# Performance work log

Measured on AMD Instinct MI355X. Metric: run time of the kernel, lower is better.

## Reference

```python
import jax, jax.numpy as jnp
import numpy as np

EPS = 1e-5
N0, K1, K2 = 1000, 500, 100  # node counts fixed by the view() calls in the source


def _conv_bn_relu(x, w, b, g, be):
    # Conv1d(k=1) == per-node linear; BatchNorm1d in training mode over nodes
    h = x @ w.T + b                      # (N, Cout)
    mu = h.mean(0)
    var = h.var(0)                       # biased variance, as torch BN uses
    return jax.nn.relu(g * (h - mu) * jax.lax.rsqrt(var + EPS) + be)


def _linear_relu(x, w, b):
    return jax.nn.relu(x @ w.T + b)


def _sag_pool(x, src, dst, ew, w_rel, w_root, bias, k):
    # SAGPooling with GraphConv scorer (sum aggregation weighted by edge_attr)
    N = x.shape[0]
    agg = jax.ops.segment_sum(ew[:, None] * x[src], dst, num_segments=N)  # (N, C)
    score = agg @ w_rel + x @ w_root + bias                               # (N,)
    top_s, perm = jax.lax.top_k(score, k)
    xk = x[perm] * jnp.tanh(top_s)[:, None]                               # (k, C)
    # re-index edges: keep only edges between surviving nodes (mask, fixed E)
    new_idx = jnp.zeros(N, jnp.int32).at[perm].set(jnp.arange(k, dtype=jnp.int32))
    keep = jnp.zeros(N, bool).at[perm].set(True)
    valid = keep[src] & keep[dst]
    nsrc = jnp.where(valid, new_idx[src], 0)
    ndst = jnp.where(valid, new_idx[dst], 0)
    new_ew = jnp.where(valid, ew, 0.0)  # zero weight == edge removed
    return xk, nsrc, ndst, new_ew


def setup_inputs() -> dict:
    key = jax.random.key(0)
    ks = jax.random.split(key, 32)
    nrm = lambda k, sh, s=0.05: jax.random.normal(k, sh, jnp.float32) * s
    E = 32000
    return {
        "x": jax.random.normal(ks[0], (1, N0, 3), jnp.float32),
        "edge_index": jax.random.randint(ks[1], (2, E), 0, N0, jnp.int32),
        "edge_attr": jax.random.uniform(ks[2], (E,), jnp.float32),
        # input: Conv1d(3,64)+BN
        "w0": nrm(ks[3], (64, 3)), "b0": jnp.zeros(64), "g0": jnp.ones(64), "be0": jnp.zeros(64),
        # mlp_first: Conv1d(64,64)+BN
        "w1": nrm(ks[4], (64, 64)), "b1": jnp.zeros(64), "g1": jnp.ones(64), "be1": jnp.zeros(64),
        # mlp_second: Conv1d(64,128)+BN, Conv1d(128,200)+BN
        "w2a": nrm(ks[5], (128, 64)), "b2a": jnp.zeros(128), "g2a": jnp.ones(128), "be2a": jnp.zeros(128),
        "w2b": nrm(ks[6], (200, 128)), "b2b": jnp.zeros(200), "g2b": jnp.ones(200), "be2b": jnp.zeros(200),
        # mlp_third: Conv1d(200,128), Conv1d(128,2) (no BN)
        "w3a": nrm(ks[7], (128, 200)), "b3a": jnp.zeros(128),
        "w3b": nrm(ks[8], (2, 128)), "b3b": jnp.zeros(2),
        # SAGPooling scorers (GraphConv(in_channels, 1))
        "p1_wrel": nrm(ks[9], (64,)), "p1_wroot": nrm(ks[10], (64,)), "p1_b": jnp.zeros(()),
        "p2_wrel": nrm(ks[11], (200,)), "p2_wroot": nrm(ks[12], (200,)), "p2_b": jnp.zeros(()),
    }


def reference(x, edge_index, edge_attr,
              w0, b0, g0, be0, w1, b1, g1, be1,
              w2a, b2a, g2a, be2a, w2b, b2b, g2b, be2b,
              w3a, b3a, w3b, b3b,
              p1_wrel, p1_wroot, p1_b, p2_wrel, p2_wroot, p2_b):
    h = x.reshape(N0, 3)
    src, dst = edge_index[0], edge_index[1]
    ew = edge_attr.reshape(-1)

    h = _conv_bn_relu(h, w0, b0, g0, be0)      # (1000, 64)
    h = _conv_bn_relu(h, w1, b1, g1, be1)      # (1000, 64)
    h, src, dst, ew = _sag_pool(h, src, dst, ew, p1_wrel, p1_wroot, p1_b, K1)

    h = _conv_bn_relu(h, w2a, b2a, g2a, be2a)  # (500, 128)
    h = _conv_bn_relu(h, w2b, b2b, g2b, be2b)  # (500, 200)
    h, src, dst, ew = _sag_pool(h, src, dst, ew, p2_wrel, p2_wroot, p2_b, K2)

    g = h.max(0)                               # global max pool over 100 nodes -> (200,)
    h3 = _linear_relu(g, w3a, b3a)             # (128,)
    out = _linear_relu(h3, w3b, b3b)           # (2,)
    return jax.nn.log_softmax(out)[None, :]    # (1, 2)
```

## Files before the change

### kernel.cpp

```cpp
#include <hip/hip_runtime.h>
#include <math.h>

#define EPS 1e-5f
#define N0 1000
#define NK1 500
#define NK2 100
#define NE 32000
#define NBLK 64

__device__ __forceinline__ float bnr(float h, float sc, float sh) {
    float v = fmaf(h, sc, sh);
    return v > 0.f ? v : 0.f;
}

__device__ __forceinline__ float aload(const float* p) {
    return __hip_atomic_load(p, __ATOMIC_RELAXED, __HIP_MEMORY_SCOPE_AGENT);
}
__device__ __forceinline__ void astore(float* p, float v) {
    __hip_atomic_store(p, v, __ATOMIC_RELAXED, __HIP_MEMORY_SCOPE_AGENT);
}
__device__ __forceinline__ int aiload(const int* p) {
    return __hip_atomic_load(p, __ATOMIC_RELAXED, __HIP_MEMORY_SCOPE_AGENT);
}
__device__ __forceinline__ void aistore(int* p, int v) {
    __hip_atomic_store(p, v, __ATOMIC_RELAXED, __HIP_MEMORY_SCOPE_AGENT);
}

__device__ __forceinline__ void gsync(unsigned* bar, unsigned k) {
    asm volatile("s_waitcnt vmcnt(0) lgkmcnt(0)" ::: "memory");
    __syncthreads();
    if (threadIdx.x == 0) {
        __hip_atomic_fetch_add(bar, 1u, __ATOMIC_RELAXED, __HIP_MEMORY_SCOPE_AGENT);
        const unsigned target = NBLK * k;
        unsigned spins = 0;
        while (__hip_atomic_load(bar, __ATOMIC_RELAXED, __HIP_MEMORY_SCOPE_AGENT) < target) {
            if (++spins > (1u << 20)) break;
            __builtin_amdgcn_s_sleep(1);
        }
    }
    __syncthreads();
}

struct Args {
    const float *x; const int *ei; const float *ea;
    const float *w0, *b0, *g0, *be0;
    const float *w1, *b1, *g1, *be1;
    const float *w2a, *b2a, *g2a, *be2a;
    const float *w2b, *b2b, *g2b, *be2b;
    const float *w3a, *b3a, *w3b, *b3b;
    const float *p1_wrel, *p1_wroot, *p1_b, *p2_wrel, *p2_wroot, *p2_b;
    float *h1, *psum1, *sc1, *t1, *xp1, *h2a, *psum2a;
    float *h2b, *psum2b, *t2, *sc2, *xp2;
    int *rk_g, *nsrc, *ndst; float *new_ew;
    unsigned *bar;
    float *out;
};

__global__ __launch_bounds__(256) void k_mega(Args a) {
    union __align__(16) SMem {
        struct { float xs[32][68], wsm[64][65], rs[256], rq[256], sc0[64], sh0[64]; } m1;
        struct { float xs[16][68], wsm[128][65], rs[256], rq[256]; } m2;
        struct { float wsm[200][33], xs[8][36], sc[128], sh[128]; } m3;
        struct { float acc[N0]; } sct;
        struct { float ss[N0], sc[200], sh[200]; } rk;
        struct { float sc[200], sh[200]; } bn;
        struct { float g[200], h3[128], o[2]; } fin;
    };
    __shared__ SMem sm;
    const int b = blockIdx.x, t = threadIdx.x;
    const int lane = t & 63, wv = t >> 6;

    if (b < 32) {
        const int c = lane, slot = wv;
        const int nb = b * 32;
        {
            float wa = a.w0[c * 3], wb = a.w0[c * 3 + 1], wc = a.w0[c * 3 + 2], bb = a.b0[c];
            float s = 0.f, q = 0.f;
            for (int n = slot; n < N0; n += 4) {
                float h = fmaf(wa, a.x[n * 3], fmaf(wb, a.x[n * 3 + 1], fmaf(wc, a.x[n * 3 + 2], bb)));
                s += h; q += h * h;
            }
            sm.m1.rs[t] = s; sm.m1.rq[t] = q;
            __syncthreads();
            if (t < 64) {
                float S = sm.m1.rs[t] + sm.m1.rs[t + 64] + sm.m1.rs[t + 128] + sm.m1.rs[t + 192];
                float Q = sm.m1.rq[t] + sm.m1.rq[t + 64] + sm.m1.rq[t + 128] + sm.m1.rq[t + 192];
                float mu = S * (1.f / N0);
                float var = Q * (1.f / N0) - mu * mu;
                float sv = a.g0[t] * rsqrtf(var + EPS);
                sm.m1.sc0[t] = sv; sm.m1.sh0[t] = a.be0[t] - mu * sv;
            }
            __syncthreads();
        }
        for (int i = 0; i < 8; ++i) {
            int e = t + i * 256;
            int r = e >> 6, cc = e & 63;
            int n = nb + r;
            float v = 0.f;
            if (n < N0) {
                float h = fmaf(a.w0[cc * 3], a.x[n * 3],
                          fmaf(a.w0[cc * 3 + 1], a.x[n * 3 + 1],
                          fmaf(a.w0[cc * 3 + 2], a.x[n * 3 + 2], a.b0[cc])));
                v = bnr(h, sm.m1.sc0[cc], sm.m1.sh0[cc]);
            }
            sm.m1.xs[r][cc] = v;
        }
        for (int i = 0; i < 16; ++i) {
            int e = t + i * 256;
            sm.m1.wsm[e >> 6][e & 63] = a.w1[e];
        }
        __syncthreads();
        float sacc = 0.f, qacc = 0.f;
        float bb1 = a.b1[c];
        for (int g = 0; g < 2; ++g) {
            int r0 = slot * 8 + g * 4;
            float a0 = bb1, a1 = bb1, a2 = bb1, a3 = bb1;
            #pragma unroll
            for (int kq = 0; kq < 16; ++kq) {
                float w0v = sm.m1.wsm[c][4 * kq], w1v = sm.m1.wsm[c][4 * kq + 1];
                float w2v = sm.m1.wsm[c][4 * kq + 2], w3v = sm.m1.wsm[c][4 * kq + 3];
                float4 x0 = *(const float4*)&sm.m1.xs[r0 + 0][4 * kq];
                float4 x1 = *(const float4*)&sm.m1.xs[r0 + 1][4 * kq];
                float4 x2 = *(const float4*)&sm.m1.xs[r0 + 2][4 * kq];
                float4 x3 = *(const float4*)&sm.m1.xs[r0 + 3][4 * kq];
                a0 = fmaf(x0.x, w0v, fmaf(x0.y, w1v, fmaf(x0.z, w2v, fmaf(x0.w, w3v, a0))));
                a1 = fmaf(x1.x, w0v, fmaf(x1.y, w1v, fmaf(x1.z, w2v, fmaf(x1.w, w3v, a1))));
                a2 = fmaf(x2.x, w0v, fmaf(x2.y, w1v, fmaf(x2.z, w2v, fmaf(x2.w, w3v, a2))));
                a3 = fmaf(x3.x, w0v, fmaf(x3.y, w1v, fmaf(x3.z, w2v, fmaf(x3.w, w3v, a3))));
            }
            float av[4] = {a0, a1, a2, a3};
            #pragma unroll
            for (int i = 0; i < 4; ++i) {
                int n = nb + r0 + i;
                if (n < N0) {
                    astore(&a.h1[n * 64 + c], av[i]);
                    sacc += av[i]; qacc += av[i] * av[i];
                }
            }
        }
        sm.m1.rs[t] = sacc; sm.m1.rq[t] = qacc;
        __syncthreads();
        if (t < 64) {
            astore(&a.psum1[b * 128 + t],      sm.m1.rs[t] + sm.m1.rs[t + 64] + sm.m1.rs[t + 128] + sm.m1.rs[t + 192]);
            astore(&a.psum1[b * 128 + 64 + t], sm.m1.rq[t] + sm.m1.rq[t + 64] + sm.m1.rq[t + 128] + sm.m1.rq[t + 192]);
        }
    }
    gsync(a.bar, 1);

    if (b < 63) {
        if (t < 64) {
            float s = 0.f, q = 0.f;
            for (int i = 0; i < 32; ++i) { s += aload(&a.psum1[i * 128 + t]); q += aload(&a.psum1[i * 128 + 64 + t]); }
            float mu = s * (1.f / N0);
            float var = q * (1.f / N0) - mu * mu;
            float sv = a.g1[t] * rsqrtf(var + EPS);
            sm.bn.sc[t] = sv; sm.bn.sh[t] = a.be1[t] - mu * sv;
        }
        __syncthreads();
        for (int it = 0; it < 4; ++it) {
            int n = b * 16 + it * 4 + wv;
            if (n < N0) {
                float v = bnr(aload(&a.h1[n * 64 + lane]), sm.bn.sc[lane], sm.bn.sh[lane]);
                float dr = v * a.p1_wrel[lane], dt = v * a.p1_wroot[lane];
                #pragma unroll
                for (int m = 32; m >= 1; m >>= 1) {
                    dr += __shfl_xor(dr, m, 64);
                    dt += __shfl_xor(dt, m, 64);
                }
                if (lane == 0) { astore(&a.t1[n], dr); astore(&a.sc1[n], dt + a.p1_b[0]); }
            }
        }
    }
    gsync(a.bar, 2);

    if (b < 16) {
        for (int i = t; i < N0; i += 256) sm.sct.acc[i] = 0.f;
        __syncthreads();
        for (int e = b * 256 + t; e < NE; e += 16 * 256) {
            float w = a.ea[e];
            if (w != 0.f) atomicAdd(&sm.sct.acc[a.ei[NE + e]], w * aload(&a.t1[a.ei[e]]));
        }
        __syncthreads();
        for (int i = t; i < N0; i += 256) {
            float v = sm.sct.acc[i];
            if (v != 0.f) atomicAdd(&a.sc1[i], v);
        }
    }
    gsync(a.bar, 3);

    if (b < 63) {
        if (t < 64) {
            float s = 0.f, q = 0.f;
            for (int i = 0; i < 32; ++i) { s += aload(&a.psum1[i * 128 + t]); q += aload(&a.psum1[i * 128 + 64 + t]); }
            float mu = s * (1.f / N0);
            float var = q * (1.f / N0) - mu * mu;
            float sv = a.g1[t] * rsqrtf(var + EPS);
            sm.rk.sc[t] = sv; sm.rk.sh[t] = a.be1[t] - mu * sv;
        }
        for (int i = t; i < N0; i += 256) sm.rk.ss[i] = aload(&a.sc1[i]);
        __syncthreads();
        for (int it = 0; it < 4; ++it) {
            int n = b * 16 + it * 4 + wv;
            if (n < N0) {
                float s = sm.rk.ss[n];
                int r = 0;
                for (int m = lane; m < N0; m += 64) {
                    float smv = sm.rk.ss[m];
                    r += (smv > s) || (smv == s && m < n);
                }
                #pragma unroll
                for (int msk = 32; msk >= 1; msk >>= 1) r += __shfl_xor(r, msk, 64);
                if (lane == 0) aistore(&a.rk_g[n], r);
                if (r < NK1) {
                    float tn = tanhf(s);
                    astore(&a.xp1[r * 64 + lane],
                           bnr(aload(&a.h1[n * 64 + lane]), sm.rk.sc[lane], sm.rk.sh[lane]) * tn);
                }
            }
        }
    }
    gsync(a.bar, 4);

    if (b < 32) {
        const int nb = b * 16;
        const int nrows = (NK1 - nb) < 16 ? (NK1 - nb) : 16;
        for (int i = 0; i < 4; ++i) {
            int e = t + i * 256;
            int r = e >> 6, cc = e & 63;
            sm.m2.xs[r][cc] = (r < nrows) ? aload(&a.xp1[(nb + r) * 64 + cc]) : 0.f;
        }
        for (int i = 0; i < 32; ++i) {
            int e = t + i * 256;
            sm.m2.wsm[e >> 6][e & 63] = a.w2a[e];
        }
        __syncthreads();
        const int c = t & 127, slot = t >> 7;
        float sacc = 0.f, qacc = 0.f;
        float bb2 = a.b2a[c];
        for (int g = 0; g < 2; ++g) {
            int r0 = slot * 8 + g * 4;
            float a0 = bb2, a1 = bb2, a2 = bb2, a3 = bb2;
            #pragma unroll
            for (int kq = 0; kq < 16; ++kq) {
                float w0v = sm.m2.wsm[c][4 * kq], w1v = sm.m2.wsm[c][4 * kq + 1];
                float w2v = sm.m2.wsm[c][4 * kq + 2], w3v = sm.m2.wsm[c][4 * kq + 3];
                float4 x0 = *(const float4*)&sm.m2.xs[r0 + 0][4 * kq];
                float4 x1 = *(const float4*)&sm.m2.xs[r0 + 1][4 * kq];
                float4 x2 = *(const float4*)&sm.m2.xs[r0 + 2][4 * kq];
                float4 x3 = *(const float4*)&sm.m2.xs[r0 + 3][4 * kq];
                a0 = fmaf(x0.x, w0v, fmaf(x0.y, w1v, fmaf(x0.z, w2v, fmaf(x0.w, w3v, a0))));
                a1 = fmaf(x1.x, w0v, fmaf(x1.y, w1v, fmaf(x1.z, w2v, fmaf(x1.w, w3v, a1))));
                a2 = fmaf(x2.x, w0v, fmaf(x2.y, w1v, fmaf(x2.z, w2v, fmaf(x2.w, w3v, a2))));
                a3 = fmaf(x3.x, w0v, fmaf(x3.y, w1v, fmaf(x3.z, w2v, fmaf(x3.w, w3v, a3))));
            }
            float av[4] = {a0, a1, a2, a3};
            #pragma unroll
            for (int i = 0; i < 4; ++i) {
                int r = r0 + i;
                if (r < nrows) {
                    astore(&a.h2a[(nb + r) * 128 + c], av[i]);
                    sacc += av[i]; qacc += av[i] * av[i];
                }
            }
        }
        sm.m2.rs[t] = sacc; sm.m2.rq[t] = qacc;
        __syncthreads();
        if (t < 128) {
            astore(&a.psum2a[b * 256 + t],       sm.m2.rs[t] + sm.m2.rs[t + 128]);
            astore(&a.psum2a[b * 256 + 128 + t], sm.m2.rq[t] + sm.m2.rq[t + 128]);
        }
    } else {
        int e0 = (b - 32) * 1000;
        for (int e = e0 + t; e < e0 + 1000; e += 256) {
            int s_ = a.ei[e], d_ = a.ei[NE + e];
            int rs_ = aiload(&a.rk_g[s_]), rd_ = aiload(&a.rk_g[d_]);
            bool v = (rs_ < NK1) && (rd_ < NK1);
            aistore(&a.nsrc[e], v ? rs_ : 0);
            aistore(&a.ndst[e], v ? rd_ : 0);
            astore(&a.new_ew[e], v ? a.ea[e] : 0.f);
        }
    }
    gsync(a.bar, 5);

    {
        const int nb = b * 8;
        if (nb < NK1) {
            const int nrows = (NK1 - nb) < 8 ? (NK1 - nb) : 8;
            if (t < 128) {
                float s = 0.f, q = 0.f;
                for (int i = 0; i < 32; ++i) { s += aload(&a.psum2a[i * 256 + t]); q += aload(&a.psum2a[i * 256 + 128 + t]); }
                float mu = s * (1.f / NK1);
                float var = q * (1.f / NK1) - mu * mu;
                float sv = a.g2a[t] * rsqrtf(var + EPS);
                sm.m3.sc[t] = sv; sm.m3.sh[t] = a.be2a[t] - mu * sv;
            }
            float acc[8];
            float bb = (t < 200) ? a.b2b[t] : 0.f;
            #pragma unroll
            for (int r = 0; r < 8; ++r) acc[r] = bb;
            for (int kt = 0; kt < 4; ++kt) {
                int k0 = kt * 32;
                __syncthreads();
                for (int i = 0; i < 25; ++i) {
                    int e = t + i * 256;
                    int r = e >> 5, k = e & 31;
                    sm.m3.wsm[r][k] = a.w2b[r * 128 + k0 + k];
                }
                {
                    int r = t >> 5, k = t & 31;
                    sm.m3.xs[r][k] = (r < nrows)
                        ? bnr(aload(&a.h2a[(nb + r) * 128 + k0 + k]), sm.m3.sc[k0 + k], sm.m3.sh[k0 + k]) : 0.f;
                }
                __syncthreads();
                if (t < 200) {
                    #pragma unroll
                    for (int kq = 0; kq < 8; ++kq) {
                        float w0v = sm.m3.wsm[t][4 * kq], w1v = sm.m3.wsm[t][4 * kq + 1];
                        float w2v = sm.m3.wsm[t][4 * kq + 2], w3v = sm.m3.wsm[t][4 * kq + 3];
                        #pragma unroll
                        for (int r = 0; r < 8; ++r) {
                            float4 xv = *(const float4*)&sm.m3.xs[r][4 * kq];
                            acc[r] = fmaf(xv.x, w0v, fmaf(xv.y, w1v, fmaf(xv.z, w2v, fmaf(xv.w, w3v, acc[r]))));
                        }
                    }
                }
            }
            if (t < 200) {
                float s = 0.f, q = 0.f;
                #pragma unroll
                for (int r = 0; r < 8; ++r) {
                    if (r < nrows) {
                        astore(&a.h2b[(nb + r) * 200 + t], acc[r]);
                        s += acc[r]; q += acc[r] * acc[r];
                    }
                }
                astore(&a.psum2b[b * 400 + t], s);
                astore(&a.psum2b[b * 400 + 200 + t], q);
            }
        } else if (t < 200) {
            astore(&a.psum2b[b * 400 + t], 0.f);
            astore(&a.psum2b[b * 400 + 200 + t], 0.f);
        }
    }
    gsync(a.bar, 6);

    if (b < 63) {
        if (t < 200) {
            float s = 0.f, q = 0.f;
            for (int i = 0; i < 64; ++i) { s += aload(&a.psum2b[i * 400 + t]); q += aload(&a.psum2b[i * 400 + 200 + t]); }
            float mu = s * (1.f / NK1);
            float var = q * (1.f / NK1) - mu * mu;
            float sv = a.g2b[t] * rsqrtf(var + EPS);
            sm.bn.sc[t] = sv; sm.bn.sh[t] = a.be2b[t] - mu * sv;
        }
        __syncthreads();
        for (int it = 0; it < 2; ++it) {
            int n = b * 8 + it * 4 + wv;
            if (n < NK1) {
                float dr = 0.f, dt = 0.f;
                #pragma unroll
                for (int j = 0; j < 4; ++j) {
                    int ch = lane + 64 * j;
                    if (ch < 200) {
                        float v = bnr(aload(&a.h2b[n * 200 + ch]), sm.bn.sc[ch], sm.bn.sh[ch]);
                        dr = fmaf(v, a.p2_wrel[ch], dr);
                        dt = fmaf(v, a.p2_wroot[ch], dt);
                    }
                }
                #pragma unroll
                for (int m = 32; m >= 1; m >>= 1) {
                    dr += __shfl_xor(dr, m, 64);
                    dt += __shfl_xor(dt, m, 64);
                }
                if (lane == 0) { astore(&a.t2[n], dr); astore(&a.sc2[n], dt + a.p2_b[0]); }
            }
        }
    }
    gsync(a.bar, 7);

    if (b < 16) {
        for (int i = t; i < NK1; i += 256) sm.sct.acc[i] = 0.f;
        __syncthreads();
        for (int e = b * 256 + t; e < NE; e += 16 * 256) {
            float w = aload(&a.new_ew[e]);
            if (w != 0.f) atomicAdd(&sm.sct.acc[aiload(&a.ndst[e])], w * aload(&a.t2[aiload(&a.nsrc[e])]));
        }
        __syncthreads();
        for (int i = t; i < NK1; i += 256) {
            float v = sm.sct.acc[i];
            if (v != 0.f) atomicAdd(&a.sc2[i], v);
        }
    }
    gsync(a.bar, 8);

    if (b < 63) {
        if (t < 200) {
            float s = 0.f, q = 0.f;
            for (int i = 0; i < 64; ++i) { s += aload(&a.psum2b[i * 400 + t]); q += aload(&a.psum2b[i * 400 + 200 + t]); }
            float mu = s * (1.f / NK1);
            float var = q * (1.f / NK1) - mu * mu;
            float sv = a.g2b[t] * rsqrtf(var + EPS);
            sm.rk.sc[t] = sv; sm.rk.sh[t] = a.be2b[t] - mu * sv;
        }
        for (int i = t; i < NK1; i += 256) sm.rk.ss[i] = aload(&a.sc2[i]);
        __syncthreads();
        for (int it = 0; it < 2; ++it) {
            int n = b * 8 + it * 4 + wv;
            if (n < NK1) {
                float s = sm.rk.ss[n];
                int r = 0;
                for (int m = lane; m < NK1; m += 64) {
                    float smv = sm.rk.ss[m];
                    r += (smv > s) || (smv == s && m < n);
                }
                #pragma unroll
                for (int msk = 32; msk >= 1; msk >>= 1) r += __shfl_xor(r, msk, 64);
                if (r < NK2) {
                    float tn = tanhf(s);
                    #pragma unroll
                    for (int j = 0; j < 4; ++j) {
                        int ch = lane + 64 * j;
                        if (ch < 200)
                            astore(&a.xp2[r * 200 + ch],
                                   bnr(aload(&a.h2b[n * 200 + ch]), sm.rk.sc[ch], sm.rk.sh[ch]) * tn);
                    }
                }
            }
        }
    }
    gsync(a.bar, 9);

    if (b == 0) {
        if (t < 200) {
            float m = -1e30f;
            for (int n = 0; n < NK2; ++n) m = fmaxf(m, aload(&a.xp2[n * 200 + t]));
            sm.fin.g[t] = m;
        }
        __syncthreads();
        for (int r = wv; r < 128; r += 4) {
            float p = 0.f;
            #pragma unroll
            for (int j = 0; j < 4; ++j) {
                int ch = lane + 64 * j;
                if (ch < 200) p = fmaf(a.w3a[r * 200 + ch], sm.fin.g[ch], p);
            }
            #pragma unroll
            for (int m = 32; m >= 1; m >>= 1) p += __shfl_xor(p, m, 64);
            if (lane == 0) sm.fin.h3[r] = fmaxf(p + a.b3a[r], 0.f);
        }
        __syncthreads();
        if (t < 128) {
            int ow = t >> 6;
            float p = a.w3b[ow * 128 + lane] * sm.fin.h3[lane]
                    + a.w3b[ow * 128 + 64 + lane] * sm.fin.h3[64 + lane];
            #pragma unroll
            for (int m = 32; m >= 1; m >>= 1) p += __shfl_xor(p, m, 64);
            if (lane == 0) sm.fin.o[ow] = fmaxf(p + a.b3b[ow], 0.f);
        }
        __syncthreads();
        if (t == 0) {
            float m = fmaxf(sm.fin.o[0], sm.fin.o[1]);
            float l = m + logf(expf(sm.fin.o[0] - m) + expf(sm.fin.o[1] - m));
            a.out[0] = sm.fin.o[0] - l;
            a.out[1] = sm.fin.o[1] - l;
        }
    }
}

extern "C" void kernel_launch(void* const* d_in, const int* in_sizes, int n_in,
                              void* d_out, int out_size, void* d_ws, size_t ws_size,
                              hipStream_t stream) {
    float* ws = (float*)d_ws;

    Args a;
    a.x    = (const float*)d_in[0];
    a.ei   = (const int*)d_in[1];
    a.ea   = (const float*)d_in[2];
    a.w0   = (const float*)d_in[3];  a.b0   = (const float*)d_in[4];
    a.g0   = (const float*)d_in[5];  a.be0  = (const float*)d_in[6];
    a.w1   = (const float*)d_in[7];  a.b1   = (const float*)d_in[8];
    a.g1   = (const float*)d_in[9];  a.be1  = (const float*)d_in[10];
    a.w2a  = (const float*)d_in[11]; a.b2a  = (const float*)d_in[12];
    a.g2a  = (const float*)d_in[13]; a.be2a = (const float*)d_in[14];
    a.w2b  = (const float*)d_in[15]; a.b2b  = (const float*)d_in[16];
    a.g2b  = (const float*)d_in[17]; a.be2b = (const float*)d_in[18];
    a.w3a  = (const float*)d_in[19]; a.b3a  = (const float*)d_in[20];
    a.w3b  = (const float*)d_in[21]; a.b3b  = (const float*)d_in[22];
    a.p1_wrel  = (const float*)d_in[23];
    a.p1_wroot = (const float*)d_in[24];
    a.p1_b     = (const float*)d_in[25];
    a.p2_wrel  = (const float*)d_in[26];
    a.p2_wroot = (const float*)d_in[27];
    a.p2_b     = (const float*)d_in[28];

    a.h1     = ws;
    a.psum1  = ws + 64000;
    a.rk_g   = (int*)(ws + 68096);
    a.sc1    = ws + 69096;
    a.t1     = ws + 70096;
    a.xp1    = ws + 71096;
    a.h2a    = ws + 103096;
    a.psum2a = ws + 167096;
    a.h2b    = ws + 175288;
    a.psum2b = ws + 275288;
    a.t2     = ws + 300888;
    a.sc2    = ws + 301388;
    a.xp2    = ws + 301888;
    a.nsrc   = (int*)(ws + 321888);
    a.ndst   = (int*)(ws + 353888);
    a.new_ew = ws + 385888;
    a.bar    = (unsigned*)(ws + 417888);
    a.out    = (float*)d_out;

    hipMemsetAsync((void*)a.bar, 0, sizeof(unsigned), stream);
    k_mega<<<NBLK, 256, 0, stream>>>(a);
}
```

Before: 127.0 us.

## Cut grid barriers by redundantly computing pool scores per block with deterministic fixed-point scatter

Every block now computes the full pooling scores and the edge scatter-add in shared memory, with the adds done as 64-bit fixed-point atomics so all blocks get bit-identical results. This removes several grid-wide barriers and the global score arrays. The final pool, max and MLP tail is fused into one block. The barrier counter moves to a persistent device global with an epoch, so the per-launch memset goes away. The cost is redundant per-block edge and score work and a fixed-point quantisation of the aggregation.

```diff
diff --git a/kernel.cpp b/kernel.cpp
--- a/kernel.cpp
+++ b/kernel.cpp
@@ -7,12 +7,16 @@
 #define NK2 100
 #define NE 32000
 #define NBLK 64
+#define NSYNC 4
+#define FPSCALE 16777216.0f
+
+__device__ unsigned g_bar = 0u;
+__device__ unsigned g_epoch = 0u;
 
 __device__ __forceinline__ float bnr(float h, float sc, float sh) {
     float v = fmaf(h, sc, sh);
     return v > 0.f ? v : 0.f;
 }
-
 __device__ __forceinline__ float aload(const float* p) {
     return __hip_atomic_load(p, __ATOMIC_RELAXED, __HIP_MEMORY_SCOPE_AGENT);
 }
@@ -26,16 +30,21 @@
     __hip_atomic_store(p, v, __ATOMIC_RELAXED, __HIP_MEMORY_SCOPE_AGENT);
 }
 
-__device__ __forceinline__ void gsync(unsigned* bar, unsigned k) {
+__device__ __forceinline__ void gsync(unsigned base, unsigned k, bool spin) {
     asm volatile("s_waitcnt vmcnt(0) lgkmcnt(0)" ::: "memory");
     __syncthreads();
     if (threadIdx.x == 0) {
-        __hip_atomic_fetch_add(bar, 1u, __ATOMIC_RELAXED, __HIP_MEMORY_SCOPE_AGENT);
-        const unsigned target = NBLK * k;
-        unsigned spins = 0;
-        while (__hip_atomic_load(bar, __ATOMIC_RELAXED, __HIP_MEMORY_SCOPE_AGENT) < target) {
-            if (++spins > (1u << 20)) break;
-            __builtin_amdgcn_s_sleep(1);
+        unsigned ret = __hip_atomic_fetch_add(&g_bar, 1u, __ATOMIC_RELAXED, __HIP_MEMORY_SCOPE_AGENT);
+        if (k == NSYNC && ret == base + NSYNC * NBLK - 1u)
+            __hip_atomic_store(&g_epoch, base / (NSYNC * NBLK) + 1u,
+                               __ATOMIC_RELAXED, __HIP_MEMORY_SCOPE_AGENT);
+        if (spin) {
+            unsigned target = base + k * NBLK;
+            unsigned spins = 0;
+            while (__hip_atomic_load(&g_bar, __ATOMIC_RELAXED, __HIP_MEMORY_SCOPE_AGENT) < target) {
+                if (++spins > (1u << 22)) break;
+                __builtin_amdgcn_s_sleep(1);
+            }
         }
     }
     __syncthreads();
@@ -49,50 +58,55 @@
     const float *w2b, *b2b, *g2b, *be2b;
     const float *w3a, *b3a, *w3b, *b3b;
     const float *p1_wrel, *p1_wroot, *p1_b, *p2_wrel, *p2_wroot, *p2_b;
-    float *h1, *psum1, *sc1, *t1, *xp1, *h2a, *psum2a;
-    float *h2b, *psum2b, *t2, *sc2, *xp2;
+    float *h1, *psum1, *xp1, *h2a, *psum2a, *h2b, *psum2b;
     int *rk_g, *nsrc, *ndst; float *new_ew;
-    unsigned *bar;
     float *out;
 };
 
 __global__ __launch_bounds__(256) void k_mega(Args a) {
     union __align__(16) SMem {
-        struct { float xs[32][68], wsm[64][65], rs[256], rq[256], sc0[64], sh0[64]; } m1;
-        struct { float xs[16][68], wsm[128][65], rs[256], rq[256]; } m2;
-        struct { float wsm[200][33], xs[8][36], sc[128], sh[128]; } m3;
-        struct { float acc[N0]; } sct;
-        struct { float ss[N0], sc[200], sh[200]; } rk;
-        struct { float sc[200], sh[200]; } bn;
-        struct { float g[200], h3[128], o[2]; } fin;
+        struct { float xs[16][68], wsm[64][65], rs[256], rq[256], sc0[64], sh0[64]; } A;
+        struct { float ss[N0], tt[N0]; unsigned long long acc64[N0];
+                 float rs[256], rq[256], sc[64], sh[64], wr[64], wo[64]; } B;
+        struct { float xs[8][68], wsm[128][65], rs[256], rq[256]; } C;
+        struct { float wsm[200][33], xs[8][36], sc[128], sh[128], rs[256], rq[256]; } D;
+        struct { float ss[NK1], tt[NK1]; unsigned long long acc64[NK1];
+                 float sc[200], sh[200], wr[200], wo[200], g[200], h3[128], o[2];
+                 int pn[NK2]; float th[NK2]; } E;
     };
     __shared__ SMem sm;
+    __shared__ unsigned sh_base;
     const int b = blockIdx.x, t = threadIdx.x;
     const int lane = t & 63, wv = t >> 6;
 
-    if (b < 32) {
-        const int c = lane, slot = wv;
-        const int nb = b * 32;
+    if (t == 0)
+        sh_base = __hip_atomic_load(&g_epoch, __ATOMIC_RELAXED, __HIP_MEMORY_SCOPE_AGENT) * (NSYNC * NBLK);
+    __syncthreads();
+    const unsigned base = sh_base;
+
+    {
+        const int nb = b * 16;
         {
+            const int c = lane, slot = wv;
             float wa = a.w0[c * 3], wb = a.w0[c * 3 + 1], wc = a.w0[c * 3 + 2], bb = a.b0[c];
             float s = 0.f, q = 0.f;
             for (int n = slot; n < N0; n += 4) {
                 float h = fmaf(wa, a.x[n * 3], fmaf(wb, a.x[n * 3 + 1], fmaf(wc, a.x[n * 3 + 2], bb)));
                 s += h; q += h * h;
             }
-            sm.m1.rs[t] = s; sm.m1.rq[t] = q;
+            sm.A.rs[t] = s; sm.A.rq[t] = q;
             __syncthreads();
             if (t < 64) {
-                float S = sm.m1.rs[t] + sm.m1.rs[t + 64] + sm.m1.rs[t + 128] + sm.m1.rs[t + 192];
-                float Q = sm.m1.rq[t] + sm.m1.rq[t + 64] + sm.m1.rq[t + 128] + sm.m1.rq[t + 192];
+                float S = sm.A.rs[t] + sm.A.rs[t + 64] + sm.A.rs[t + 128] + sm.A.rs[t + 192];
+                float Q = sm.A.rq[t] + sm.A.rq[t + 64] + sm.A.rq[t + 128] + sm.A.rq[t + 192];
                 float mu = S * (1.f / N0);
                 float var = Q * (1.f / N0) - mu * mu;
                 float sv = a.g0[t] * rsqrtf(var + EPS);
-                sm.m1.sc0[t] = sv; sm.m1.sh0[t] = a.be0[t] - mu * sv;
+                sm.A.sc0[t] = sv; sm.A.sh0[t] = a.be0[t] - mu * sv;
             }
             __syncthreads();
         }
-        for (int i = 0; i < 8; ++i) {
+        for (int i = 0; i < 4; ++i) {
             int e = t + i * 256;
             int r = e >> 6, cc = e & 63;
             int n = nb + r;
@@ -101,111 +115,127 @@
                 float h = fmaf(a.w0[cc * 3], a.x[n * 3],
                           fmaf(a.w0[cc * 3 + 1], a.x[n * 3 + 1],
                           fmaf(a.w0[cc * 3 + 2], a.x[n * 3 + 2], a.b0[cc])));
-                v = bnr(h, sm.m1.sc0[cc], sm.m1.sh0[cc]);
-            }
-            sm.m1.xs[r][cc] = v;
+                v = bnr(h, sm.A.sc0[cc], sm.A.sh0[cc]);
+            }
+            sm.A.xs[r][cc] = v;
         }
         for (int i = 0; i < 16; ++i) {
             int e = t + i * 256;
-            sm.m1.wsm[e >> 6][e & 63] = a.w1[e];
-        }
-        __syncthreads();
+            sm.A.wsm[e >> 6][e & 63] = a.w1[e];
+        }
+        __syncthreads();
+        const int c = lane, slot = wv;
+        const int r0 = slot * 4;
+        float bb1 = a.b1[c];
+        float a0 = bb1, a1 = bb1, a2 = bb1, a3 = bb1;
+        #pragma unroll
+        for (int kq = 0; kq < 16; ++kq) {
+            float w0v = sm.A.wsm[c][4 * kq],     w1v = sm.A.wsm[c][4 * kq + 1];
+            float w2v = sm.A.wsm[c][4 * kq + 2], w3v = sm.A.wsm[c][4 * kq + 3];
+            float4 x0 = *(const float4*)&sm.A.xs[r0 + 0][4 * kq];
+            float4 x1 = *(const float4*)&sm.A.xs[r0 + 1][4 * kq];
+            float4 x2 = *(const float4*)&sm.A.xs[r0 + 2][4 * kq];
+            float4 x3 = *(const float4*)&sm.A.xs[r0 + 3][4 * kq];
+            a0 = fmaf(x0.x, w0v, fmaf(x0.y, w1v, fmaf(x0.z, w2v, fmaf(x0.w, w3v, a0))));
+            a1 = fmaf(x1.x, w0v, fmaf(x1.y, w1v, fmaf(x1.z, w2v, fmaf(x1.w, w3v, a1))));
+            a2 = fmaf(x2.x, w0v, fmaf(x2.y, w1v, fmaf(x2.z, w2v, fmaf(x2.w, w3v, a2))));
+            a3 = fmaf(x3.x, w0v, fmaf(x3.y, w1v, fmaf(x3.z, w2v, fmaf(x3.w, w3v, a3))));
+        }
+        float av[4] = {a0, a1, a2, a3};
         float sacc = 0.f, qacc = 0.f;
-        float bb1 = a.b1[c];
-        for (int g = 0; g < 2; ++g) {
-            int r0 = slot * 8 + g * 4;
-            float a0 = bb1, a1 = bb1, a2 = bb1, a3 = bb1;
+        #pragma unroll
+        for (int i = 0; i < 4; ++i) {
+            int n = nb + r0 + i;
+            if (n < N0) {
+                astore(&a.h1[n * 64 + c], av[i]);
+                sacc += av[i]; qacc += av[i] * av[i];
+            }
+        }
+        __syncthreads();
+        sm.A.rs[t] = sacc; sm.A.rq[t] = qacc;
+        __syncthreads();
+        if (t < 64) {
+            astore(&a.psum1[b * 128 + t],
+                   sm.A.rs[t] + sm.A.rs[t + 64] + sm.A.rs[t + 128] + sm.A.rs[t + 192]);
+            astore(&a.psum1[b * 128 + 64 + t],
+                   sm.A.rq[t] + sm.A.rq[t + 64] + sm.A.rq[t + 128] + sm.A.rq[t + 192]);
+        }
+    }
+    gsync(base, 1, true);
+
+    {
+        {
+            const int ch = t & 63, part = t >> 6;
+            float s = 0.f, q = 0.f;
+            for (int i = 0; i < 16; ++i) {
+                int blk = part * 16 + i;
+                s += aload(&a.psum1[blk * 128 + ch]);
+                q += aload(&a.psum1[blk * 128 + 64 + ch]);
+            }
+            sm.B.rs[t] = s; sm.B.rq[t] = q;
+        }
+        for (int i = t; i < N0; i += 256) sm.B.acc64[i] = 0ull;
+        if (t < 64) { sm.B.wr[t] = a.p1_wrel[t]; sm.B.wo[t] = a.p1_wroot[t]; }
+        __syncthreads();
+        if (t < 64) {
+            float S = sm.B.rs[t] + sm.B.rs[t + 64] + sm.B.rs[t + 128] + sm.B.rs[t + 192];
+            float Q = sm.B.rq[t] + sm.B.rq[t + 64] + sm.B.rq[t + 128] + sm.B.rq[t + 192];
+            float mu = S * (1.f / N0);
+            float var = Q * (1.f / N0) - mu * mu;
+            float sv = a.g1[t] * rsqrtf(var + EPS);
+            sm.B.sc[t] = sv; sm.B.sh[t] = a.be1[t] - mu * sv;
+        }
+        __syncthreads();
+
+        {
+            const int sub = t & 3, grp = t >> 2;
+            float wrv[16], wov[16], scv[16], shv[16];
             #pragma unroll
-            for (int kq = 0; kq < 16; ++kq) {
-                float w0v = sm.m1.wsm[c][4 * kq], w1v = sm.m1.wsm[c][4 * kq + 1];
-                float w2v = sm.m1.wsm[c][4 * kq + 2], w3v = sm.m1.wsm[c][4 * kq + 3];
-                float4 x0 = *(const float4*)&sm.m1.xs[r0 + 0][4 * kq];
-                float4 x1 = *(const float4*)&sm.m1.xs[r0 + 1][4 * kq];
-                float4 x2 = *(const float4*)&sm.m1.xs[r0 + 2][4 * kq];
-                float4 x3 = *(const float4*)&sm.m1.xs[r0 + 3][4 * kq];
-                a0 = fmaf(x0.x, w0v, fmaf(x0.y, w1v, fmaf(x0.z, w2v, fmaf(x0.w, w3v, a0))));
-                a1 = fmaf(x1.x, w0v, fmaf(x1.y, w1v, fmaf(x1.z, w2v, fmaf(x1.w, w3v, a1))));
-                a2 = fmaf(x2.x, w0v, fmaf(x2.y, w1v, fmaf(x2.z, w2v, fmaf(x2.w, w3v, a2))));
-                a3 = fmaf(x3.x, w0v, fmaf(x3.y, w1v, fmaf(x3.z, w2v, fmaf(x3.w, w3v, a3))));
-            }
-            float av[4] = {a0, a1, a2, a3};
-            #pragma unroll
-            for (int i = 0; i < 4; ++i) {
-                int n = nb + r0 + i;
+            for (int i = 0; i < 16; ++i) {
+                int ch = sub * 16 + i;
+                wrv[i] = sm.B.wr[ch]; wov[i] = sm.B.wo[ch];
+                scv[i] = sm.B.sc[ch]; shv[i] = sm.B.sh[ch];
+            }
+            float pb = a.p1_b[0];
+            for (int p = 0; p < 16; ++p) {
+                int n = p * 64 + grp;
                 if (n < N0) {
-                    astore(&a.h1[n * 64 + c], av[i]);
-                    sacc += av[i]; qacc += av[i] * av[i];
-                }
-            }
-        }
-        sm.m1.rs[t] = sacc; sm.m1.rq[t] = qacc;
-        __syncthreads();
-        if (t < 64) {
-            astore(&a.psum1[b * 128 + t],      sm.m1.rs[t] + sm.m1.rs[t + 64] + sm.m1.rs[t + 128] + sm.m1.rs[t + 192]);
-            astore(&a.psum1[b * 128 + 64 + t], sm.m1.rq[t] + sm.m1.rq[t + 64] + sm.m1.rq[t + 128] + sm.m1.rq[t + 192]);
-        }
-    }
-    gsync(a.bar, 1);
-
-    if (b < 63) {
-        if (t < 64) {
-            float s = 0.f, q = 0.f;
-            for (int i = 0; i < 32; ++i) { s += aload(&a.psum1[i * 128 + t]); q += aload(&a.psum1[i * 128 + 64 + t]); }
-            float mu = s * (1.f / N0);
-            float var = q * (1.f / N0) - mu * mu;
-            float sv = a.g1[t] * rsqrtf(var + EPS);
-            sm.bn.sc[t] = sv; sm.bn.sh[t] = a.be1[t] - mu * sv;
-        }
-        __syncthreads();
+                    float dr = 0.f, dt = 0.f;
+                    #pragma unroll
+                    for (int i = 0; i < 16; ++i) {
+                        float v = bnr(aload(&a.h1[n * 64 + sub * 16 + i]), scv[i], shv[i]);
+                        dr = fmaf(v, wrv[i], dr);
+                        dt = fmaf(v, wov[i], dt);
+                    }
+                    dr += __shfl_xor(dr, 1, 64); dr += __shfl_xor(dr, 2, 64);
+                    dt += __shfl_xor(dt, 1, 64); dt += __shfl_xor(dt, 2, 64);
+                    if (sub == 0) { sm.B.tt[n] = dr; sm.B.ss[n] = dt + pb; }
+                }
+            }
+        }
+        __syncthreads();
+
+        for (int e = t; e < NE; e += 256) {
+            float w = a.ea[e];
+            if (w != 0.f) {
+                float c = w * sm.B.tt[a.ei[e]];
+                long long ll = __float2ll_rn(c * FPSCALE);
+                atomicAdd((unsigned long long*)&sm.B.acc64[a.ei[NE + e]],
+                          (unsigned long long)ll);
+            }
+        }
+        __syncthreads();
+        for (int i = t; i < N0; i += 256)
+            sm.B.ss[i] += (float)((double)(long long)sm.B.acc64[i] * (1.0 / (double)FPSCALE));
+        __syncthreads();
+
         for (int it = 0; it < 4; ++it) {
             int n = b * 16 + it * 4 + wv;
             if (n < N0) {
-                float v = bnr(aload(&a.h1[n * 64 + lane]), sm.bn.sc[lane], sm.bn.sh[lane]);
-                float dr = v * a.p1_wrel[lane], dt = v * a.p1_wroot[lane];
-                #pragma unroll
-                for (int m = 32; m >= 1; m >>= 1) {
-                    dr += __shfl_xor(dr, m, 64);
-                    dt += __shfl_xor(dt, m, 64);
-                }
-                if (lane == 0) { astore(&a.t1[n], dr); astore(&a.sc1[n], dt + a.p1_b[0]); }
-            }
-        }
-    }
-    gsync(a.bar, 2);
-
-    if (b < 16) {
-        for (int i = t; i < N0; i += 256) sm.sct.acc[i] = 0.f;
-        __syncthreads();
-        for (int e = b * 256 + t; e < NE; e += 16 * 256) {
-            float w = a.ea[e];
-            if (w != 0.f) atomicAdd(&sm.sct.acc[a.ei[NE + e]], w * aload(&a.t1[a.ei[e]]));
-        }
-        __syncthreads();
-        for (int i = t; i < N0; i += 256) {
-            float v = sm.sct.acc[i];
-            if (v != 0.f) atomicAdd(&a.sc1[i], v);
-        }
-    }
-    gsync(a.bar, 3);
-
-    if (b < 63) {
-        if (t < 64) {
-            float s = 0.f, q = 0.f;
-            for (int i = 0; i < 32; ++i) { s += aload(&a.psum1[i * 128 + t]); q += aload(&a.psum1[i * 128 + 64 + t]); }
-            float mu = s * (1.f / N0);
-            float var = q * (1.f / N0) - mu * mu;
-            float sv = a.g1[t] * rsqrtf(var + EPS);
-            sm.rk.sc[t] = sv; sm.rk.sh[t] = a.be1[t] - mu * sv;
-        }
-        for (int i = t; i < N0; i += 256) sm.rk.ss[i] = aload(&a.sc1[i]);
-        __syncthreads();
-        for (int it = 0; it < 4; ++it) {
-            int n = b * 16 + it * 4 + wv;
-            if (n < N0) {
-                float s = sm.rk.ss[n];
+                float s = sm.B.ss[n];
                 int r = 0;
                 for (int m = lane; m < N0; m += 64) {
-                    float smv = sm.rk.ss[m];
+                    float smv = sm.B.ss[m];
                     r += (smv > s) || (smv == s && m < n);
                 }
                 #pragma unroll
@@ -214,64 +244,17 @@
                 if (r < NK1) {
                     float tn = tanhf(s);
                     astore(&a.xp1[r * 64 + lane],
-                           bnr(aload(&a.h1[n * 64 + lane]), sm.rk.sc[lane], sm.rk.sh[lane]) * tn);
+                           bnr(aload(&a.h1[n * 64 + lane]), sm.B.sc[lane], sm.B.sh[lane]) * tn);
                 }
             }
         }
     }
-    gsync(a.bar, 4);
-
-    if (b < 32) {
-        const int nb = b * 16;
-        const int nrows = (NK1 - nb) < 16 ? (NK1 - nb) : 16;
-        for (int i = 0; i < 4; ++i) {
-            int e = t + i * 256;
-            int r = e >> 6, cc = e & 63;
-            sm.m2.xs[r][cc] = (r < nrows) ? aload(&a.xp1[(nb + r) * 64 + cc]) : 0.f;
-        }
-        for (int i = 0; i < 32; ++i) {
-            int e = t + i * 256;
-            sm.m2.wsm[e >> 6][e & 63] = a.w2a[e];
-        }
-        __syncthreads();
-        const int c = t & 127, slot = t >> 7;
-        float sacc = 0.f, qacc = 0.f;
-        float bb2 = a.b2a[c];
-        for (int g = 0; g < 2; ++g) {
-            int r0 = slot * 8 + g * 4;
-            float a0 = bb2, a1 = bb2, a2 = bb2, a3 = bb2;
-            #pragma unroll
-            for (int kq = 0; kq < 16; ++kq) {
-                float w0v = sm.m2.wsm[c][4 * kq], w1v = sm.m2.wsm[c][4 * kq + 1];
-                float w2v = sm.m2.wsm[c][4 * kq + 2], w3v = sm.m2.wsm[c][4 * kq + 3];
-                float4 x0 = *(const float4*)&sm.m2.xs[r0 + 0][4 * kq];
-                float4 x1 = *(const float4*)&sm.m2.xs[r0 + 1][4 * kq];
-                float4 x2 = *(const float4*)&sm.m2.xs[r0 + 2][4 * kq];
-                float4 x3 = *(const float4*)&sm.m2.xs[r0 + 3][4 * kq];
-                a0 = fmaf(x0.x, w0v, fmaf(x0.y, w1v, fmaf(x0.z, w2v, fmaf(x0.w, w3v, a0))));
-                a1 = fmaf(x1.x, w0v, fmaf(x1.y, w1v, fmaf(x1.z, w2v, fmaf(x1.w, w3v, a1))));
-                a2 = fmaf(x2.x, w0v, fmaf(x2.y, w1v, fmaf(x2.z, w2v, fmaf(x2.w, w3v, a2))));
-                a3 = fmaf(x3.x, w0v, fmaf(x3.y, w1v, fmaf(x3.z, w2v, fmaf(x3.w, w3v, a3))));
-            }
-            float av[4] = {a0, a1, a2, a3};
-            #pragma unroll
-            for (int i = 0; i < 4; ++i) {
-                int r = r0 + i;
-                if (r < nrows) {
-                    astore(&a.h2a[(nb + r) * 128 + c], av[i]);
-                    sacc += av[i]; qacc += av[i] * av[i];
-                }
-            }
-        }
-        sm.m2.rs[t] = sacc; sm.m2.rq[t] = qacc;
-        __syncthreads();
-        if (t < 128) {
-            astore(&a.psum2a[b * 256 + t],       sm.m2.rs[t] + sm.m2.rs[t + 128]);
-            astore(&a.psum2a[b * 256 + 128 + t], sm.m2.rq[t] + sm.m2.rq[t + 128]);
-        }
-    } else {
-        int e0 = (b - 32) * 1000;
-        for (int e = e0 + t; e < e0 + 1000; e += 256) {
+    gsync(base, 2, true);
+
+    {
+        const int nb = b * 8;
+        const int nrows = (NK1 - nb) < 8 ? ((NK1 - nb) > 0 ? (NK1 - nb) : 0) : 8;
+        for (int e = b * 500 + t; e < b * 500 + 500; e += 256) {
             int s_ = a.ei[e], d_ = a.ei[NE + e];
             int rs_ = aiload(&a.rk_g[s_]), rd_ = aiload(&a.rk_g[d_]);
             bool v = (rs_ < NK1) && (rd_ < NK1);
@@ -279,190 +262,225 @@
             aistore(&a.ndst[e], v ? rd_ : 0);
             astore(&a.new_ew[e], v ? a.ea[e] : 0.f);
         }
+        for (int i = 0; i < 2; ++i) {
+            int e = t + i * 256;
+            int r = e >> 6, cc = e & 63;
+            sm.C.xs[r][cc] = (r < nrows) ? aload(&a.xp1[(nb + r) * 64 + cc]) : 0.f;
+        }
+        for (int i = 0; i < 32; ++i) {
+            int e = t + i * 256;
+            sm.C.wsm[e >> 6][e & 63] = a.w2a[e];
+        }
+        __syncthreads();
+        const int c = t & 127, half = t >> 7;
+        const int r0 = half * 4;
+        float bb2 = a.b2a[c];
+        float a0 = bb2, a1 = bb2, a2 = bb2, a3 = bb2;
+        #pragma unroll
+        for (int kq = 0; kq < 16; ++kq) {
+            float w0v = sm.C.wsm[c][4 * kq],     w1v = sm.C.wsm[c][4 * kq + 1];
+            float w2v = sm.C.wsm[c][4 * kq + 2], w3v = sm.C.wsm[c][4 * kq + 3];
+            float4 x0 = *(const float4*)&sm.C.xs[r0 + 0][4 * kq];
+            float4 x1 = *(const float4*)&sm.C.xs[r0 + 1][4 * kq];
+            float4 x2 = *(const float4*)&sm.C.xs[r0 + 2][4 * kq];
+            float4 x3 = *(const float4*)&sm.C.xs[r0 + 3][4 * kq];
+            a0 = fmaf(x0.x, w0v, fmaf(x0.y, w1v, fmaf(x0.z, w2v, fmaf(x0.w, w3v, a0))));
+            a1 = fmaf(x1.x, w0v, fmaf(x1.y, w1v, fmaf(x1.z, w2v, fmaf(x1.w, w3v, a1))));
+            a2 = fmaf(x2.x, w0v, fmaf(x2.y, w1v, fmaf(x2.z, w2v, fmaf(x2.w, w3v, a2))));
+            a3 = fmaf(x3.x, w0v, fmaf(x3.y, w1v, fmaf(x3.z, w2v, fmaf(x3.w, w3v, a3))));
+        }
+        float av[4] = {a0, a1, a2, a3};
+        float sacc = 0.f, qacc = 0.f;
+        #pragma unroll
+        for (int i = 0; i < 4; ++i) {
+            int r = r0 + i;
+            if (r < nrows) {
+                astore(&a.h2a[(nb + r) * 128 + c], av[i]);
+                sacc += av[i]; qacc += av[i] * av[i];
+            }
+        }
+        __syncthreads();
+        sm.C.rs[t] = sacc; sm.C.rq[t] = qacc;
+        __syncthreads();
+        if (t < 128) {
+            astore(&a.psum2a[b * 256 + t],       sm.C.rs[t] + sm.C.rs[t + 128]);
+            astore(&a.psum2a[b * 256 + 128 + t], sm.C.rq[t] + sm.C.rq[t + 128]);
+        }
     }
-    gsync(a.bar, 5);
+    gsync(base, 3, true);
 
     {
         const int nb = b * 8;
-        if (nb < NK1) {
-            const int nrows = (NK1 - nb) < 8 ? (NK1 - nb) : 8;
-            if (t < 128) {
-                float s = 0.f, q = 0.f;
-                for (int i = 0; i < 32; ++i) { s += aload(&a.psum2a[i * 256 + t]); q += aload(&a.psum2a[i * 256 + 128 + t]); }
-                float mu = s * (1.f / NK1);
-                float var = q * (1.f / NK1) - mu * mu;
-                float sv = a.g2a[t] * rsqrtf(var + EPS);
-                sm.m3.sc[t] = sv; sm.m3.sh[t] = a.be2a[t] - mu * sv;
-            }
-            float acc[8];
-            float bb = (t < 200) ? a.b2b[t] : 0.f;
-            #pragma unroll
-            for (int r = 0; r < 8; ++r) acc[r] = bb;
-            for (int kt = 0; kt < 4; ++kt) {
-                int k0 = kt * 32;
-                __syncthreads();
-                for (int i = 0; i < 25; ++i) {
-                    int e = t + i * 256;
-                    int r = e >> 5, k = e & 31;
-                    sm.m3.wsm[r][k] = a.w2b[r * 128 + k0 + k];
-                }
-                {
-                    int r = t >> 5, k = t & 31;
-                    sm.m3.xs[r][k] = (r < nrows)
-                        ? bnr(aload(&a.h2a[(nb + r) * 128 + k0 + k]), sm.m3.sc[k0 + k], sm.m3.sh[k0 + k]) : 0.f;
-                }
-                __syncthreads();
-                if (t < 200) {
+        const int nrows = (NK1 - nb) < 8 ? ((NK1 - nb) > 0 ? (NK1 - nb) : 0) : 8;
+        {
+            const int ch = t & 127, half = t >> 7;
+            float s = 0.f, q = 0.f;
+            for (int i = 0; i < 32; ++i) {
+                int blk = half * 32 + i;
+                s += aload(&a.psum2a[blk * 256 + ch]);
+                q += aload(&a.psum2a[blk * 256 + 128 + ch]);
+            }
+            sm.D.rs[t] = s; sm.D.rq[t] = q;
+        }
+        __syncthreads();
+        if (t < 128) {
+            float S = sm.D.rs[t] + sm.D.rs[t + 128];
+            float Q = sm.D.rq[t] + sm.D.rq[t + 128];
+            float mu = S * (1.f / NK1);
+            float var = Q * (1.f / NK1) - mu * mu;
+            float sv = a.g2a[t] * rsqrtf(var + EPS);
+            sm.D.sc[t] = sv; sm.D.sh[t] = a.be2a[t] - mu * sv;
+        }
+        float acc[8];
+        float bb = (t < 200) ? a.b2b[t] : 0.f;
+        #pragma unroll
+        for (int r = 0; r < 8; ++r) acc[r] = bb;
+        for (int kt = 0; kt < 4; ++kt) {
+            int k0 = kt * 32;
+            __syncthreads();
+            for (int i = 0; i < 25; ++i) {
+                int e = t + i * 256;
+                int r = e >> 5, k = e & 31;
+                sm.D.wsm[r][k] = a.w2b[r * 128 + k0 + k];
+            }
+            {
+                int r = t >> 5, k = t & 31;
+                sm.D.xs[r][k] = (r < nrows)
+                    ? bnr(aload(&a.h2a[(nb + r) * 128 + k0 + k]), sm.D.sc[k0 + k], sm.D.sh[k0 + k])
+                    : 0.f;
+            }
+            __syncthreads();
+            if (t < 200) {
+                #pragma unroll
+                for (int kq = 0; kq < 8; ++kq) {
+                    float w0v = sm.D.wsm[t][4 * kq],     w1v = sm.D.wsm[t][4 * kq + 1];
+                    float w2v = sm.D.wsm[t][4 * kq + 2], w3v = sm.D.wsm[t][4 * kq + 3];
                     #pragma unroll
-                    for (int kq = 0; kq < 8; ++kq) {
-                        float w0v = sm.m3.wsm[t][4 * kq], w1v = sm.m3.wsm[t][4 * kq + 1];
-                        float w2v = sm.m3.wsm[t][4 * kq + 2], w3v = sm.m3.wsm[t][4 * kq + 3];
-                        #pragma unroll
-                        for (int r = 0; r < 8; ++r) {
-                            float4 xv = *(const float4*)&sm.m3.xs[r][4 * kq];
-                            acc[r] = fmaf(xv.x, w0v, fmaf(xv.y, w1v, fmaf(xv.z, w2v, fmaf(xv.w, w3v, acc[r]))));
-                        }
+                    for (int r = 0; r < 8; ++r) {
+                        float4 xv = *(const float4*)&sm.D.xs[r][4 * kq];
+                        acc[r] = fmaf(xv.x, w0v, fmaf(xv.y, w1v, fmaf(xv.z, w2v, fmaf(xv.w, w3v, acc[r]))));
                     }
                 }
             }
-            if (t < 200) {
-                float s = 0.f, q = 0.f;
-                #pragma unroll
-                for (int r = 0; r < 8; ++r) {
-                    if (r < nrows) {
-                        astore(&a.h2b[(nb + r) * 200 + t], acc[r]);
-                        s += acc[r]; q += acc[r] * acc[r];
-                    }
-                }
-                astore(&a.psum2b[b * 400 + t], s);
-                astore(&a.psum2b[b * 400 + 200 + t], q);
-            }
-        } else if (t < 200) {
-            astore(&a.psum2b[b * 400 + t], 0.f);
-            astore(&a.psum2b[b * 400 + 200 + t], 0.f);
-        }
-    }
-    gsync(a.bar, 6);
-
-    if (b < 63) {
+        }
         if (t < 200) {
             float s = 0.f, q = 0.f;
-            for (int i = 0; i < 64; ++i) { s += aload(&a.psum2b[i * 400 + t]); q += aload(&a.psum2b[i * 400 + 200 + t]); }
+            #pragma unroll
+            for (int r = 0; r < 8; ++r) {
+                if (r < nrows) {
+                    astore(&a.h2b[(nb + r) * 200 + t], acc[r]);
+                    s += acc[r]; q += acc[r] * acc[r];
+                }
+            }
+            astore(&a.psum2b[b * 400 + t], s);
+            astore(&a.psum2b[b * 400 + 200 + t], q);
+        }
+    }
+    gsync(base, 4, b == 0);
+
+    if (b == 0) {
+        if (t < 200) {
+            float s = 0.f, q = 0.f;
+            for (int i = 0; i < 64; ++i) {
+                s += aload(&a.psum2b[i * 400 + t]);
+                q += aload(&a.psum2b[i * 400 + 200 + t]);
+            }
             float mu = s * (1.f / NK1);
             float var = q * (1.f / NK1) - mu * mu;
             float sv = a.g2b[t] * rsqrtf(var + EPS);
-            sm.bn.sc[t] = sv; sm.bn.sh[t] = a.be2b[t] - mu * sv;
-        }
-        __syncthreads();
-        for (int it = 0; it < 2; ++it) {
-            int n = b * 8 + it * 4 + wv;
-            if (n < NK1) {
-                float dr = 0.f, dt = 0.f;
-                #pragma unroll
-                for (int j = 0; j < 4; ++j) {
-                    int ch = lane + 64 * j;
-                    if (ch < 200) {
-                        float v = bnr(aload(&a.h2b[n * 200 + ch]), sm.bn.sc[ch], sm.bn.sh[ch]);
-                        dr = fmaf(v, a.p2_wrel[ch], dr);
-                        dt = fmaf(v, a.p2_wroot[ch], dt);
+            sm.E.sc[t] = sv; sm.E.sh[t] = a.be2b[t] - mu * sv;
+            sm.E.wr[t] = a.p2_wrel[t]; sm.E.wo[t] = a.p2_wroot[t];
+        }
+        for (int i = t; i < NK1; i += 256) sm.E.acc64[i] = 0ull;
+        __syncthreads();
+
+        {
+            const int sub = t & 3, grp = t >> 2;
+            float pb2 = a.p2_b[0];
+            for (int p = 0; p < 8; ++p) {
+                int n = p * 64 + grp;
+                if (n < NK1) {
+                    float dr = 0.f, dt = 0.f;
+                    for (int i = 0; i < 50; ++i) {
+                        int ch = sub * 50 + i;
+                        float v = bnr(aload(&a.h2b[n * 200 + ch]), sm.E.sc[ch], sm.E.sh[ch]);
+                        dr = fmaf(v, sm.E.wr[ch], dr);
+                        dt = fmaf(v, sm.E.wo[ch], dt);
                     }
-                }
-                #pragma unroll
-                for (int m = 32; m >= 1; m >>= 1) {
-                    dr += __shfl_xor(dr, m, 64);
-                    dt += __shfl_xor(dt, m, 64);
-                }
-                if (lane == 0) { astore(&a.t2[n], dr); astore(&a.sc2[n], dt + a.p2_b[0]); }
-            }
-        }
-    }
-    gsync(a.bar, 7);
-
-    if (b < 16) {
-        for (int i = t; i < NK1; i += 256) sm.sct.acc[i] = 0.f;
-        __syncthreads();
-        for (int e = b * 256 + t; e < NE; e += 16 * 256) {
+                    dr += __shfl_xor(dr, 1, 64); dr += __shfl_xor(dr, 2, 64);
+                    dt += __shfl_xor(dt, 1, 64); dt += __shfl_xor(dt, 2, 64);
+                    if (sub == 0) { sm.E.tt[n] = dr; sm.E.ss[n] = dt + pb2; }
+                }
+            }
+        }
+        __syncthreads();
+
+        for (int e = t; e < NE; e += 256) {
             float w = aload(&a.new_ew[e]);
-            if (w != 0.f) atomicAdd(&sm.sct.acc[aiload(&a.ndst[e])], w * aload(&a.t2[aiload(&a.nsrc[e])]));
-        }
-        __syncthreads();
-        for (int i = t; i < NK1; i += 256) {
-            float v = sm.sct.acc[i];
-            if (v != 0.f) atomicAdd(&a.sc2[i], v);
-        }
-    }
-    gsync(a.bar, 8);
-
-    if (b < 63) {
-        if (t < 200) {
-            float s = 0.f, q = 0.f;
-            for (int i = 0; i < 64; ++i) { s += aload(&a.psum2b[i * 400 + t]); q += aload(&a.psum2b[i * 400 + 200 + t]); }
-            float mu = s * (1.f / NK1);
-            float var = q * (1.f / NK1) - mu * mu;
-            float sv = a.g2b[t] * rsqrtf(var + EPS);
-            sm.rk.sc[t] = sv; sm.rk.sh[t] = a.be2b[t] - mu * sv;
-        }
-        for (int i = t; i < NK1; i += 256) sm.rk.ss[i] = aload(&a.sc2[i]);
-        __syncthreads();
-        for (int it = 0; it < 2; ++it) {
-            int n = b * 8 + it * 4 + wv;
-            if (n < NK1) {
-                float s = sm.rk.ss[n];
+            if (w != 0.f) {
+                float c = w * sm.E.tt[aiload(&a.nsrc[e])];
+                long long ll = __float2ll_rn(c * FPSCALE);
+                atomicAdd((unsigned long long*)&sm.E.acc64[aiload(&a.ndst[e])],
+                          (unsigned long long)ll);
+            }
+        }
+        __syncthreads();
+        for (int i = t; i < NK1; i += 256)
+            sm.E.ss[i] += (float)((double)(long long)sm.E.acc64[i] * (1.0 / (double)FPSCALE));
+        __syncthreads();
+
+        if (t < 250) {
+            #pragma unroll
+            for (int h = 0; h < 2; ++h) {
+                int n = t + h * 250;
+                float s = sm.E.ss[n];
                 int r = 0;
-                for (int m = lane; m < NK1; m += 64) {
-                    float smv = sm.rk.ss[m];
+                for (int m = 0; m < NK1; ++m) {
+                    float smv = sm.E.ss[m];
                     r += (smv > s) || (smv == s && m < n);
                 }
-                #pragma unroll
-                for (int msk = 32; msk >= 1; msk >>= 1) r += __shfl_xor(r, msk, 64);
-                if (r < NK2) {
-                    float tn = tanhf(s);
-                    #pragma unroll
-                    for (int j = 0; j < 4; ++j) {
-                        int ch = lane + 64 * j;
-                        if (ch < 200)
-                            astore(&a.xp2[r * 200 + ch],
-                                   bnr(aload(&a.h2b[n * 200 + ch]), sm.rk.sc[ch], sm.rk.sh[ch]) * tn);
-                    }
-                }
-            }
-        }
-    }
-    gsync(a.bar, 9);
-
-    if (b == 0) {
+                if (r < NK2) { sm.E.pn[r] = n; sm.E.th[r] = tanhf(s); }
+            }
+        }
+        __syncthreads();
+
         if (t < 200) {
             float m = -1e30f;
-            for (int n = 0; n < NK2; ++n) m = fmaxf(m, aload(&a.xp2[n * 200 + t]));
-            sm.fin.g[t] = m;
-        }
-        __syncthreads();
-        for (int r = wv; r < 128; r += 4) {
+            for (int j = 0; j < NK2; ++j) {
+                float v = bnr(aload(&a.h2b[sm.E.pn[j] * 200 + t]), sm.E.sc[t], sm.E.sh[t]) * sm.E.th[j];
+                m = fmaxf(m, v);
+            }
+            sm.E.g[t] = m;
+        }
+        __syncthreads();
+
+        for (int i = 0; i < 32; ++i) {
+            int r = wv + 4 * i;
             float p = 0.f;
             #pragma unroll
             for (int j = 0; j < 4; ++j) {
                 int ch = lane + 64 * j;
-                if (ch < 200) p = fmaf(a.w3a[r * 200 + ch], sm.fin.g[ch], p);
+                if (ch < 200) p = fmaf(a.w3a[r * 200 + ch], sm.E.g[ch], p);
             }
             #pragma unroll
             for (int m = 32; m >= 1; m >>= 1) p += __shfl_xor(p, m, 64);
-            if (lane == 0) sm.fin.h3[r] = fmaxf(p + a.b3a[r], 0.f);
+            if (lane == 0) sm.E.h3[r] = fmaxf(p + a.b3a[r], 0.f);
         }
         __syncthreads();
         if (t < 128) {
             int ow = t >> 6;
-            float p = a.w3b[ow * 128 + lane] * sm.fin.h3[lane]
-                    + a.w3b[ow * 128 + 64 + lane] * sm.fin.h3[64 + lane];
+            float p = a.w3b[ow * 128 + lane] * sm.E.h3[lane]
+                    + a.w3b[ow * 128 + 64 + lane] * sm.E.h3[64 + lane];
             #pragma unroll
             for (int m = 32; m >= 1; m >>= 1) p += __shfl_xor(p, m, 64);
-            if (lane == 0) sm.fin.o[ow] = fmaxf(p + a.b3b[ow], 0.f);
+            if (lane == 0) sm.E.o[ow] = fmaxf(p + a.b3b[ow], 0.f);
         }
         __syncthreads();
         if (t == 0) {
-            float m = fmaxf(sm.fin.o[0], sm.fin.o[1]);
-            float l = m + logf(expf(sm.fin.o[0] - m) + expf(sm.fin.o[1] - m));
-            a.out[0] = sm.fin.o[0] - l;
-            a.out[1] = sm.fin.o[1] - l;
+            float m = fmaxf(sm.E.o[0], sm.E.o[1]);
+            float l = m + logf(expf(sm.E.o[0] - m) + expf(sm.E.o[1] - m));
+            a.out[0] = sm.E.o[0] - l;
+            a.out[1] = sm.E.o[1] - l;
         }
     }
 }
@@ -495,23 +513,16 @@
 
     a.h1     = ws;
     a.psum1  = ws + 64000;
-    a.rk_g   = (int*)(ws + 68096);
-    a.sc1    = ws + 69096;
-    a.t1     = ws + 70096;
-    a.xp1    = ws + 71096;
-    a.h2a    = ws + 103096;
-    a.psum2a = ws + 167096;
-    a.h2b    = ws + 175288;
-    a.psum2b = ws + 275288;
-    a.t2     = ws + 300888;
-    a.sc2    = ws + 301388;
-    a.xp2    = ws + 301888;
-    a.nsrc   = (int*)(ws + 321888);
-    a.ndst   = (int*)(ws + 353888);
-    a.new_ew = ws + 385888;
-    a.bar    = (unsigned*)(ws + 417888);
+    a.xp1    = ws + 72192;
+    a.rk_g   = (int*)(ws + 104192);
+    a.h2a    = ws + 105192;
+    a.psum2a = ws + 169192;
+    a.h2b    = ws + 185576;
+    a.psum2b = ws + 285576;
+    a.nsrc   = (int*)(ws + 311176);
+    a.ndst   = (int*)(ws + 343176);
+    a.new_ew = ws + 375176;
     a.out    = (float*)d_out;
 
-    hipMemsetAsync((void*)a.bar, 0, sizeof(unsigned), stream);
     k_mega<<<NBLK, 256, 0, stream>>>(a);
 }
```

After: 335.1 us. 2.64x slower.
